# Kernel tuning notes

Hardware: AMD Instinct MI355X
Metric: run time of the kernel (lower is better)

Reference implementation:

```python
import jax, jax.numpy as jnp
import numpy as np

QUERY_SIZE = 512
KEY_SIZE = 512
VALUE_SIZE = 512
HIDDEN = 128


def setup_inputs() -> dict:
    key = jax.random.key(0)
    ks = jax.random.split(key, 9)
    b, t_q, t_k = 8, 128, 512
    query = jax.random.normal(ks[0], (b, t_q, QUERY_SIZE), dtype=jnp.float32)
    keys = jax.random.normal(ks[1], (b, t_k, KEY_SIZE), dtype=jnp.float32)
    values = jax.random.normal(ks[2], (b, t_k, VALUE_SIZE), dtype=jnp.float32)
    # torch nn.Linear init ~ U(-1/sqrt(fan_in), 1/sqrt(fan_in)); scale-matched normals are fine
    sq = 1.0 / np.sqrt(QUERY_SIZE)
    sk = 1.0 / np.sqrt(KEY_SIZE)
    sh = 1.0 / np.sqrt(HIDDEN)
    Wq = jax.random.uniform(ks[3], (HIDDEN, QUERY_SIZE), jnp.float32, -sq, sq)
    bq = jax.random.uniform(ks[4], (HIDDEN,), jnp.float32, -sq, sq)
    Wk = jax.random.uniform(ks[5], (HIDDEN, KEY_SIZE), jnp.float32, -sk, sk)
    bk = jax.random.uniform(ks[6], (HIDDEN,), jnp.float32, -sk, sk)
    Wo = jax.random.uniform(ks[7], (1, HIDDEN), jnp.float32, -sh, sh)
    bo = jax.random.uniform(ks[8], (1,), jnp.float32, -sh, sh)
    return {"query": query, "keys": keys, "values": values,
            "Wq": Wq, "bq": bq, "Wk": Wk, "bk": bk, "Wo": Wo, "bo": bo}


def reference(query, keys, values, Wq, bq, Wk, bk, Wo, bo):
    # Bahdanau additive attention: att_ij = Wo @ tanh(Wq q_i + Wk k_j + bq + bk) + bo
    # Project once per position (mathematically identical to the expanded per-pair Linear).
    q_proj = jnp.einsum('bqn,hn->bqh', query, Wq) + bq          # b x t_q x h
    k_proj = jnp.einsum('bkn,hn->bkh', keys, Wk) + bk           # b x t_k x h
    hid = jnp.tanh(q_proj[:, :, None, :] + k_proj[:, None, :, :])  # b x t_q x t_k x h
    scores = jnp.einsum('bqkh,h->bqk', hid, Wo[0]) + bo[0]       # b x t_q x t_k
    attn = jax.nn.softmax(scores, axis=2)
    context = jnp.einsum('bqk,bkv->bqv', attn, values)           # b x t_q x n_v
    return context, attn
```

## Files before the change

kernel.cpp:

```cpp
#include <hip/hip_runtime.h>


#define B_    8
#define TQ_   128
#define TK_   512
#define NIN_  512
#define H_    128
#define NV_   512
#define NQR   (B_*TQ_)
#define NROWS (NQR + B_*TK_)
#define CTXN  (B_*TQ_*NV_)

#define C2_   2.8853900817779268f
#define L2E_  1.4426950408889634f

__device__ __forceinline__ float fexp2(float x){ return __builtin_amdgcn_exp2f(x); }
__device__ __forceinline__ float frcp (float x){ return __builtin_amdgcn_rcpf(x); }

__global__ __launch_bounds__(256, 5) void proj_kernel(
        const float* __restrict__ query, const float* __restrict__ keys,
        const float* __restrict__ Wq, const float* __restrict__ Wk,
        float* __restrict__ psum, int kper) {
    __shared__ float at[32][18];
    __shared__ float wt[32][132];
    const int tid = threadIdx.x;
    const int r0  = blockIdx.x * 16;
    const float* in; const float* W;
    if (r0 < NQR) { in = query + (size_t)r0 * NIN_;         W = Wq; }
    else          { in = keys  + (size_t)(r0 - NQR) * NIN_; W = Wk; }

    const int r2 = (tid >> 5) * 2;
    const int h4 = (tid & 31) * 4;
    const int ar  = tid >> 4;
    const int ak2 = (tid & 15) * 2;
    const int wr  = tid >> 3;
    const int wkq = (tid & 7) * 4;
    const int kb0 = blockIdx.y * kper;
    const int nc  = kper >> 5;

    const float* pA  = in + (size_t)ar * NIN_ + kb0 + ak2;
    const float* pW0 = W + (size_t)(wr     ) * NIN_ + kb0 + wkq;
    const float* pW1 = W + (size_t)(wr + 32) * NIN_ + kb0 + wkq;
    const float* pW2 = W + (size_t)(wr + 64) * NIN_ + kb0 + wkq;
    const float* pW3 = W + (size_t)(wr + 96) * NIN_ + kb0 + wkq;

    float2 af = *(const float2*)pA;
    float4 w0 = *(const float4*)pW0, w1 = *(const float4*)pW1;
    float4 w2 = *(const float4*)pW2, w3 = *(const float4*)pW3;

    float acc[2][4] = {{0.f,0.f,0.f,0.f},{0.f,0.f,0.f,0.f}};

    for (int c = 0; c < nc; ++c) {
        __syncthreads();
        at[ak2+0][ar] = af.x; at[ak2+1][ar] = af.y;
        wt[wkq+0][wr   ] = w0.x; wt[wkq+1][wr   ] = w0.y;
        wt[wkq+2][wr   ] = w0.z; wt[wkq+3][wr   ] = w0.w;
        wt[wkq+0][wr+32] = w1.x; wt[wkq+1][wr+32] = w1.y;
        wt[wkq+2][wr+32] = w1.z; wt[wkq+3][wr+32] = w1.w;
        wt[wkq+0][wr+64] = w2.x; wt[wkq+1][wr+64] = w2.y;
        wt[wkq+2][wr+64] = w2.z; wt[wkq+3][wr+64] = w2.w;
        wt[wkq+0][wr+96] = w3.x; wt[wkq+1][wr+96] = w3.y;
        wt[wkq+2][wr+96] = w3.z; wt[wkq+3][wr+96] = w3.w;
        __syncthreads();
        if (c + 1 < nc) {
            pA += 32; pW0 += 32; pW1 += 32; pW2 += 32; pW3 += 32;
            af = *(const float2*)pA;
            w0 = *(const float4*)pW0; w1 = *(const float4*)pW1;
            w2 = *(const float4*)pW2; w3 = *(const float4*)pW3;
        }
#pragma unroll 8
        for (int kk = 0; kk < 32; ++kk) {
            const float2 a = *(const float2*)&at[kk][r2];
            const float4 w = *(const float4*)&wt[kk][h4];
            acc[0][0] = fmaf(a.x, w.x, acc[0][0]);
            acc[0][1] = fmaf(a.x, w.y, acc[0][1]);
            acc[0][2] = fmaf(a.x, w.z, acc[0][2]);
            acc[0][3] = fmaf(a.x, w.w, acc[0][3]);
            acc[1][0] = fmaf(a.y, w.x, acc[1][0]);
            acc[1][1] = fmaf(a.y, w.y, acc[1][1]);
            acc[1][2] = fmaf(a.y, w.z, acc[1][2]);
            acc[1][3] = fmaf(a.y, w.w, acc[1][3]);
        }
    }

    float* op = psum + ((size_t)blockIdx.y * NROWS + r0) * H_;
#pragma unroll
    for (int i = 0; i < 2; ++i) {
        float4 o = {acc[i][0], acc[i][1], acc[i][2], acc[i][3]};
        *(float4*)&op[(size_t)(r2 + i) * H_ + h4] = o;
    }
}

__global__ __launch_bounds__(256, 4) void reduceP_kernel(
        const float* __restrict__ psum, const float* __restrict__ bq,
        const float* __restrict__ bk, float* __restrict__ pout) {
    const int tid = threadIdx.x;
    const int r0  = blockIdx.x * 8;
    const float* bias = (r0 < NQR) ? bq : bk;
    const int row = tid >> 5, hq = (tid & 31) * 4;
    float4 s = *(const float4*)&bias[hq];
#pragma unroll
    for (int sp = 0; sp < 4; ++sp) {
        float4 v = *(const float4*)&psum[((size_t)sp * NROWS + r0 + row) * H_ + hq];
        s.x += v.x; s.y += v.y; s.z += v.z; s.w += v.w;
    }
    float4 o = {fexp2(s.x * C2_), fexp2(s.y * C2_),
                fexp2(s.z * C2_), fexp2(s.w * C2_)};
    *(float4*)&pout[(size_t)(r0 + row) * H_ + hq] = o;
}

__global__ __launch_bounds__(256, 4) void scores_kernel(
        const float* __restrict__ qe, const float* __restrict__ ke,
        const float* __restrict__ Wo, const float* __restrict__ bo,
        float* __restrict__ out_attn) {
    __shared__ float qs[2][H_];
    __shared__ float w2[H_];
    __shared__ float sc[2][TK_];

    const int tid = threadIdx.x;
    const int b   = blockIdx.y;
    const int q0  = blockIdx.x * 2;
    const int lane = tid & 63;

    qs[tid >> 7][tid & 127] =
        qe[(size_t)(b * TQ_ + q0 + (tid >> 7)) * H_ + (tid & 127)];
    if (tid < H_) w2[tid] = Wo[tid] * -2.0f;
    __syncthreads();

    float sw = w2[lane] + w2[lane + 64];
#pragma unroll
    for (int m = 1; m < 64; m <<= 1) sw += __shfl_xor(sw, m);
    const float sbase = bo[0] - 0.5f * sw;

#pragma unroll
    for (int half = 0; half < 2; ++half) {
        const int k = tid + half * 256;
        const float4* ke4 = (const float4*)&ke[(size_t)(b * TK_ + k) * H_];
        float s0 = 0.f, s1 = 0.f;
#pragma unroll 4
        for (int hb = 0; hb < 32; ++hb) {
            const float4 ek  = ke4[hb];
            const float4 wv  = *(const float4*)&w2[hb * 4];
            const float4 q0v = *(const float4*)&qs[0][hb * 4];
            const float4 q1v = *(const float4*)&qs[1][hb * 4];
            s0 = fmaf(wv.x, frcp(fmaf(q0v.x, ek.x, 1.f)), s0);
            s0 = fmaf(wv.y, frcp(fmaf(q0v.y, ek.y, 1.f)), s0);
            s0 = fmaf(wv.z, frcp(fmaf(q0v.z, ek.z, 1.f)), s0);
            s0 = fmaf(wv.w, frcp(fmaf(q0v.w, ek.w, 1.f)), s0);
            s1 = fmaf(wv.x, frcp(fmaf(q1v.x, ek.x, 1.f)), s1);
            s1 = fmaf(wv.y, frcp(fmaf(q1v.y, ek.y, 1.f)), s1);
            s1 = fmaf(wv.z, frcp(fmaf(q1v.z, ek.z, 1.f)), s1);
            s1 = fmaf(wv.w, frcp(fmaf(q1v.w, ek.w, 1.f)), s1);
        }
        sc[0][k] = s0 + sbase;
        sc[1][k] = s1 + sbase;
    }
    __syncthreads();

    const int w = tid >> 6;
    if (w < 2) {
        float4 sA = *(const float4*)&sc[w][lane * 8];
        float4 sB = *(const float4*)&sc[w][lane * 8 + 4];
        float m = fmaxf(fmaxf(fmaxf(sA.x, sA.y), fmaxf(sA.z, sA.w)),
                        fmaxf(fmaxf(sB.x, sB.y), fmaxf(sB.z, sB.w)));
#pragma unroll
        for (int mk = 1; mk < 64; mk <<= 1) m = fmaxf(m, __shfl_xor(m, mk));
        float4 eA, eB;
        eA.x = fexp2((sA.x - m) * L2E_); eA.y = fexp2((sA.y - m) * L2E_);
        eA.z = fexp2((sA.z - m) * L2E_); eA.w = fexp2((sA.w - m) * L2E_);
        eB.x = fexp2((sB.x - m) * L2E_); eB.y = fexp2((sB.y - m) * L2E_);
        eB.z = fexp2((sB.z - m) * L2E_); eB.w = fexp2((sB.w - m) * L2E_);
        float s = eA.x + eA.y + eA.z + eA.w + eB.x + eB.y + eB.z + eB.w;
#pragma unroll
        for (int mk = 1; mk < 64; mk <<= 1) s += __shfl_xor(s, mk);
        const float inv = frcp(s);
        eA.x *= inv; eA.y *= inv; eA.z *= inv; eA.w *= inv;
        eB.x *= inv; eB.y *= inv; eB.z *= inv; eB.w *= inv;
        float4* op = (float4*)&out_attn[(size_t)(b * TQ_ + q0 + w) * TK_ + lane * 8];
        op[0] = eA; op[1] = eB;
    }
}

__global__ __launch_bounds__(128, 4) void context_kernel(
        const float* __restrict__ attn, const float* __restrict__ values,
        float* __restrict__ psumC) {
    __shared__ float at[32][18];
    __shared__ float vt[32][68];

    const int tid = threadIdx.x;
    const int r0  = blockIdx.x * 16;
    const int b   = r0 >> 7;
    const int v0  = blockIdx.y * 64;
    const int kb0 = blockIdx.z * 128;

    const int q2 = (tid >> 4) * 2;
    const int v4 = (tid & 15) * 4;
    const int ar  = tid >> 3;
    const int akq = (tid & 7) * 4;
    const int vr  = tid >> 4;
    const int vq  = (tid & 15) * 4;

    const float* pAt = attn + (size_t)(r0 + ar) * TK_ + kb0 + akq;
    const float* pV0 = values + (size_t)(b * TK_ + kb0 + vr     ) * NV_ + v0 + vq;
    const float* pV1 = values + (size_t)(b * TK_ + kb0 + vr +  8) * NV_ + v0 + vq;
    const float* pV2 = values + (size_t)(b * TK_ + kb0 + vr + 16) * NV_ + v0 + vq;
    const float* pV3 = values + (size_t)(b * TK_ + kb0 + vr + 24) * NV_ + v0 + vq;

    float4 af  = *(const float4*)pAt;
    float4 vf0 = *(const float4*)pV0;
    float4 vf1 = *(const float4*)pV1;
    float4 vf2 = *(const float4*)pV2;
    float4 vf3 = *(const float4*)pV3;

    float acc[2][4] = {{0.f,0.f,0.f,0.f},{0.f,0.f,0.f,0.f}};

    for (int c = 0; c < 4; ++c) {
        __syncthreads();
        at[akq+0][ar] = af.x; at[akq+1][ar] = af.y;
        at[akq+2][ar] = af.z; at[akq+3][ar] = af.w;
        *(float4*)&vt[vr     ][vq] = vf0;
        *(float4*)&vt[vr +  8][vq] = vf1;
        *(float4*)&vt[vr + 16][vq] = vf2;
        *(float4*)&vt[vr + 24][vq] = vf3;
        __syncthreads();
        if (c + 1 < 4) {
            pAt += 32; pV0 += 32 * NV_; pV1 += 32 * NV_;
            pV2 += 32 * NV_; pV3 += 32 * NV_;
            af  = *(const float4*)pAt;
            vf0 = *(const float4*)pV0; vf1 = *(const float4*)pV1;
            vf2 = *(const float4*)pV2; vf3 = *(const float4*)pV3;
        }
#pragma unroll 8
        for (int kk = 0; kk < 32; ++kk) {
            const float2 a = *(const float2*)&at[kk][q2];
            const float4 v = *(const float4*)&vt[kk][v4];
            acc[0][0] = fmaf(a.x, v.x, acc[0][0]);
            acc[0][1] = fmaf(a.x, v.y, acc[0][1]);
            acc[0][2] = fmaf(a.x, v.z, acc[0][2]);
            acc[0][3] = fmaf(a.x, v.w, acc[0][3]);
            acc[1][0] = fmaf(a.y, v.x, acc[1][0]);
            acc[1][1] = fmaf(a.y, v.y, acc[1][1]);
            acc[1][2] = fmaf(a.y, v.z, acc[1][2]);
            acc[1][3] = fmaf(a.y, v.w, acc[1][3]);
        }
    }

    float* op = psumC + (size_t)blockIdx.z * CTXN + (size_t)r0 * NV_ + v0;
#pragma unroll
    for (int i = 0; i < 2; ++i) {
        float4 o = {acc[i][0], acc[i][1], acc[i][2], acc[i][3]};
        *(float4*)&op[(size_t)(q2 + i) * NV_ + v4] = o;
    }
}

__global__ __launch_bounds__(256, 4) void reduceC_kernel(
        const float* __restrict__ psumC, float* __restrict__ outc) {
    const size_t i = ((size_t)blockIdx.x * 256 + threadIdx.x) * 4;
    float4 s = *(const float4*)&psumC[i];
#pragma unroll
    for (int z = 1; z < 4; ++z) {
        float4 v = *(const float4*)&psumC[(size_t)z * CTXN + i];
        s.x += v.x; s.y += v.y; s.z += v.z; s.w += v.w;
    }
    *(float4*)&outc[i] = s;
}

extern "C" void kernel_launch(void* const* d_in, const int* in_sizes, int n_in,
                              void* d_out, int out_size, void* d_ws, size_t ws_size,
                              hipStream_t stream) {
    const float* query  = (const float*)d_in[0];
    const float* keys   = (const float*)d_in[1];
    const float* values = (const float*)d_in[2];
    const float* Wq     = (const float*)d_in[3];
    const float* bq     = (const float*)d_in[4];
    const float* Wk     = (const float*)d_in[5];
    const float* bk     = (const float*)d_in[6];
    const float* Wo     = (const float*)d_in[7];
    const float* bo     = (const float*)d_in[8];

    float* out_ctx  = (float*)d_out;
    float* out_attn = out_ctx + B_ * TQ_ * NV_;
    float* pout  = (float*)d_ws;
    float* qe    = pout;
    float* ke    = pout + (size_t)NQR * H_;
    float* psumP = pout + (size_t)NROWS * H_;
    float* psumC = psumP + (size_t)4 * NROWS * H_;

    proj_kernel<<<dim3(NROWS / 16, 4), 256, 0, stream>>>(
        query, keys, Wq, Wk, psumP, NIN_ / 4);
    reduceP_kernel<<<NROWS / 8, 256, 0, stream>>>(psumP, bq, bk, pout);
    scores_kernel<<<dim3(TQ_ / 2, B_), 256, 0, stream>>>(qe, ke, Wo, bo, out_attn);
    context_kernel<<<dim3(NQR / 16, NV_ / 64, 4), 128, 0, stream>>>(
        out_attn, values, psumC);
    reduceC_kernel<<<CTXN / 1024, 256, 0, stream>>>(psumC, out_ctx);
}
```

Baseline: 63.45 us.

## Enlarge proj register tile and split scores to one query per block

The projection GEMM now runs 128 threads per block. Each thread computes a 4x4 output tile instead of 2x4, and loads float4 from both A and W, which raises arithmetic intensity per shared-memory load. The scores kernel now handles one query per block with twice as many blocks. Each thread scores two keys with vector accumulators, and the softmax uses a block-wide reduction through a small shared array instead of a staged score buffer. The extra blocks add parallelism, but ke rows are now reread per query, since keys are no longer shared across two queries.

```diff
diff --git a/kernel.cpp b/kernel.cpp
--- a/kernel.cpp
+++ b/kernel.cpp
@@ -17,11 +17,11 @@
 __device__ __forceinline__ float fexp2(float x){ return __builtin_amdgcn_exp2f(x); }
 __device__ __forceinline__ float frcp (float x){ return __builtin_amdgcn_rcpf(x); }
 
-__global__ __launch_bounds__(256, 5) void proj_kernel(
+__global__ __launch_bounds__(128, 4) void proj_kernel(
         const float* __restrict__ query, const float* __restrict__ keys,
         const float* __restrict__ Wq, const float* __restrict__ Wk,
         float* __restrict__ psum, int kper) {
-    __shared__ float at[32][18];
+    __shared__ float at[32][20];
     __shared__ float wt[32][132];
     const int tid = threadIdx.x;
     const int r0  = blockIdx.x * 16;
@@ -29,65 +29,84 @@
     if (r0 < NQR) { in = query + (size_t)r0 * NIN_;         W = Wq; }
     else          { in = keys  + (size_t)(r0 - NQR) * NIN_; W = Wk; }
 
-    const int r2 = (tid >> 5) * 2;
+    const int r4 = (tid >> 5) * 4;
     const int h4 = (tid & 31) * 4;
-    const int ar  = tid >> 4;
-    const int ak2 = (tid & 15) * 2;
-    const int wr  = tid >> 3;
-    const int wkq = (tid & 7) * 4;
+    const int sr  = tid >> 3;
+    const int skq = (tid & 7) * 4;
     const int kb0 = blockIdx.y * kper;
     const int nc  = kper >> 5;
 
-    const float* pA  = in + (size_t)ar * NIN_ + kb0 + ak2;
-    const float* pW0 = W + (size_t)(wr     ) * NIN_ + kb0 + wkq;
-    const float* pW1 = W + (size_t)(wr + 32) * NIN_ + kb0 + wkq;
-    const float* pW2 = W + (size_t)(wr + 64) * NIN_ + kb0 + wkq;
-    const float* pW3 = W + (size_t)(wr + 96) * NIN_ + kb0 + wkq;
-
-    float2 af = *(const float2*)pA;
+    const float* pA  = in + (size_t)sr * NIN_ + kb0 + skq;
+    const float* pW0 = W + (size_t)(sr      ) * NIN_ + kb0 + skq;
+    const float* pW1 = W + (size_t)(sr + 16 ) * NIN_ + kb0 + skq;
+    const float* pW2 = W + (size_t)(sr + 32 ) * NIN_ + kb0 + skq;
+    const float* pW3 = W + (size_t)(sr + 48 ) * NIN_ + kb0 + skq;
+    const float* pW4 = W + (size_t)(sr + 64 ) * NIN_ + kb0 + skq;
+    const float* pW5 = W + (size_t)(sr + 80 ) * NIN_ + kb0 + skq;
+    const float* pW6 = W + (size_t)(sr + 96 ) * NIN_ + kb0 + skq;
+    const float* pW7 = W + (size_t)(sr + 112) * NIN_ + kb0 + skq;
+
+    float4 af = *(const float4*)pA;
     float4 w0 = *(const float4*)pW0, w1 = *(const float4*)pW1;
     float4 w2 = *(const float4*)pW2, w3 = *(const float4*)pW3;
-
-    float acc[2][4] = {{0.f,0.f,0.f,0.f},{0.f,0.f,0.f,0.f}};
+    float4 w4 = *(const float4*)pW4, w5 = *(const float4*)pW5;
+    float4 w6 = *(const float4*)pW6, w7 = *(const float4*)pW7;
+
+    float acc[4][4];
+#pragma unroll
+    for (int i = 0; i < 4; ++i)
+#pragma unroll
+        for (int j = 0; j < 4; ++j) acc[i][j] = 0.0f;
 
     for (int c = 0; c < nc; ++c) {
         __syncthreads();
-        at[ak2+0][ar] = af.x; at[ak2+1][ar] = af.y;
-        wt[wkq+0][wr   ] = w0.x; wt[wkq+1][wr   ] = w0.y;
-        wt[wkq+2][wr   ] = w0.z; wt[wkq+3][wr   ] = w0.w;
-        wt[wkq+0][wr+32] = w1.x; wt[wkq+1][wr+32] = w1.y;
-        wt[wkq+2][wr+32] = w1.z; wt[wkq+3][wr+32] = w1.w;
-        wt[wkq+0][wr+64] = w2.x; wt[wkq+1][wr+64] = w2.y;
-        wt[wkq+2][wr+64] = w2.z; wt[wkq+3][wr+64] = w2.w;
-        wt[wkq+0][wr+96] = w3.x; wt[wkq+1][wr+96] = w3.y;
-        wt[wkq+2][wr+96] = w3.z; wt[wkq+3][wr+96] = w3.w;
+        at[skq+0][sr] = af.x; at[skq+1][sr] = af.y;
+        at[skq+2][sr] = af.z; at[skq+3][sr] = af.w;
+        wt[skq+0][sr    ] = w0.x; wt[skq+1][sr    ] = w0.y;
+        wt[skq+2][sr    ] = w0.z; wt[skq+3][sr    ] = w0.w;
+        wt[skq+0][sr+ 16] = w1.x; wt[skq+1][sr+ 16] = w1.y;
+        wt[skq+2][sr+ 16] = w1.z; wt[skq+3][sr+ 16] = w1.w;
+        wt[skq+0][sr+ 32] = w2.x; wt[skq+1][sr+ 32] = w2.y;
+        wt[skq+2][sr+ 32] = w2.z; wt[skq+3][sr+ 32] = w2.w;
+        wt[skq+0][sr+ 48] = w3.x; wt[skq+1][sr+ 48] = w3.y;
+        wt[skq+2][sr+ 48] = w3.z; wt[skq+3][sr+ 48] = w3.w;
+        wt[skq+0][sr+ 64] = w4.x; wt[skq+1][sr+ 64] = w4.y;
+        wt[skq+2][sr+ 64] = w4.z; wt[skq+3][sr+ 64] = w4.w;
+        wt[skq+0][sr+ 80] = w5.x; wt[skq+1][sr+ 80] = w5.y;
+        wt[skq+2][sr+ 80] = w5.z; wt[skq+3][sr+ 80] = w5.w;
+        wt[skq+0][sr+ 96] = w6.x; wt[skq+1][sr+ 96] = w6.y;
+        wt[skq+2][sr+ 96] = w6.z; wt[skq+3][sr+ 96] = w6.w;
+        wt[skq+0][sr+112] = w7.x; wt[skq+1][sr+112] = w7.y;
+        wt[skq+2][sr+112] = w7.z; wt[skq+3][sr+112] = w7.w;
         __syncthreads();
         if (c + 1 < nc) {
             pA += 32; pW0 += 32; pW1 += 32; pW2 += 32; pW3 += 32;
-            af = *(const float2*)pA;
+            pW4 += 32; pW5 += 32; pW6 += 32; pW7 += 32;
+            af = *(const float4*)pA;
             w0 = *(const float4*)pW0; w1 = *(const float4*)pW1;
             w2 = *(const float4*)pW2; w3 = *(const float4*)pW3;
+            w4 = *(const float4*)pW4; w5 = *(const float4*)pW5;
+            w6 = *(const float4*)pW6; w7 = *(const float4*)pW7;
         }
 #pragma unroll 8
         for (int kk = 0; kk < 32; ++kk) {
-            const float2 a = *(const float2*)&at[kk][r2];
+            const float4 a = *(const float4*)&at[kk][r4];
             const float4 w = *(const float4*)&wt[kk][h4];
-            acc[0][0] = fmaf(a.x, w.x, acc[0][0]);
-            acc[0][1] = fmaf(a.x, w.y, acc[0][1]);
-            acc[0][2] = fmaf(a.x, w.z, acc[0][2]);
-            acc[0][3] = fmaf(a.x, w.w, acc[0][3]);
-            acc[1][0] = fmaf(a.y, w.x, acc[1][0]);
-            acc[1][1] = fmaf(a.y, w.y, acc[1][1]);
-            acc[1][2] = fmaf(a.y, w.z, acc[1][2]);
-            acc[1][3] = fmaf(a.y, w.w, acc[1][3]);
+            const float av[4] = {a.x, a.y, a.z, a.w};
+            const float wv[4] = {w.x, w.y, w.z, w.w};
+#pragma unroll
+            for (int i = 0; i < 4; ++i)
+#pragma unroll
+                for (int j = 0; j < 4; ++j)
+                    acc[i][j] = fmaf(av[i], wv[j], acc[i][j]);
         }
     }
 
     float* op = psum + ((size_t)blockIdx.y * NROWS + r0) * H_;
 #pragma unroll
-    for (int i = 0; i < 2; ++i) {
+    for (int i = 0; i < 4; ++i) {
         float4 o = {acc[i][0], acc[i][1], acc[i][2], acc[i][3]};
-        *(float4*)&op[(size_t)(r2 + i) * H_ + h4] = o;
+        *(float4*)&op[(size_t)(r4 + i) * H_ + h4] = o;
     }
 }
 
@@ -113,18 +132,18 @@
         const float* __restrict__ qe, const float* __restrict__ ke,
         const float* __restrict__ Wo, const float* __restrict__ bo,
         float* __restrict__ out_attn) {
-    __shared__ float qs[2][H_];
+    __shared__ float qs[H_];
     __shared__ float w2[H_];
-    __shared__ float sc[2][TK_];
-
-    const int tid = threadIdx.x;
-    const int b   = blockIdx.y;
-    const int q0  = blockIdx.x * 2;
+    __shared__ float red[8];
+
+    const int tid  = threadIdx.x;
+    const int b    = blockIdx.y;
+    const int q    = blockIdx.x;
     const int lane = tid & 63;
-
-    qs[tid >> 7][tid & 127] =
-        qe[(size_t)(b * TQ_ + q0 + (tid >> 7)) * H_ + (tid & 127)];
-    if (tid < H_) w2[tid] = Wo[tid] * -2.0f;
+    const int w    = tid >> 6;
+
+    if (tid < 128) qs[tid] = qe[(size_t)(b * TQ_ + q) * H_ + tid];
+    else           w2[tid - 128] = Wo[tid - 128] * -2.0f;
     __syncthreads();
 
     float sw = w2[lane] + w2[lane + 64];
@@ -132,53 +151,47 @@
     for (int m = 1; m < 64; m <<= 1) sw += __shfl_xor(sw, m);
     const float sbase = bo[0] - 0.5f * sw;
 
-#pragma unroll
-    for (int half = 0; half < 2; ++half) {
-        const int k = tid + half * 256;
-        const float4* ke4 = (const float4*)&ke[(size_t)(b * TK_ + k) * H_];
-        float s0 = 0.f, s1 = 0.f;
+    const float4* ke0 = (const float4*)&ke[(size_t)(b * TK_ + tid      ) * H_];
+    const float4* ke1 = (const float4*)&ke[(size_t)(b * TK_ + tid + 256) * H_];
+    float4 a0 = {0.f,0.f,0.f,0.f}, a1 = {0.f,0.f,0.f,0.f};
 #pragma unroll 4
-        for (int hb = 0; hb < 32; ++hb) {
-            const float4 ek  = ke4[hb];
-            const float4 wv  = *(const float4*)&w2[hb * 4];
-            const float4 q0v = *(const float4*)&qs[0][hb * 4];
-            const float4 q1v = *(const float4*)&qs[1][hb * 4];
-            s0 = fmaf(wv.x, frcp(fmaf(q0v.x, ek.x, 1.f)), s0);
-            s0 = fmaf(wv.y, frcp(fmaf(q0v.y, ek.y, 1.f)), s0);
-            s0 = fmaf(wv.z, frcp(fmaf(q0v.z, ek.z, 1.f)), s0);
-            s0 = fmaf(wv.w, frcp(fmaf(q0v.w, ek.w, 1.f)), s0);
-            s1 = fmaf(wv.x, frcp(fmaf(q1v.x, ek.x, 1.f)), s1);
-            s1 = fmaf(wv.y, frcp(fmaf(q1v.y, ek.y, 1.f)), s1);
-            s1 = fmaf(wv.z, frcp(fmaf(q1v.z, ek.z, 1.f)), s1);
-            s1 = fmaf(wv.w, frcp(fmaf(q1v.w, ek.w, 1.f)), s1);
-        }
-        sc[0][k] = s0 + sbase;
-        sc[1][k] = s1 + sbase;
-    }
+    for (int hb = 0; hb < 32; ++hb) {
+        const float4 e0 = ke0[hb];
+        const float4 e1 = ke1[hb];
+        const float4 wv = *(const float4*)&w2[hb * 4];
+        const float4 qv = *(const float4*)&qs[hb * 4];
+        a0.x = fmaf(wv.x, frcp(fmaf(qv.x, e0.x, 1.f)), a0.x);
+        a0.y = fmaf(wv.y, frcp(fmaf(qv.y, e0.y, 1.f)), a0.y);
+        a0.z = fmaf(wv.z, frcp(fmaf(qv.z, e0.z, 1.f)), a0.z);
+        a0.w = fmaf(wv.w, frcp(fmaf(qv.w, e0.w, 1.f)), a0.w);
+        a1.x = fmaf(wv.x, frcp(fmaf(qv.x, e1.x, 1.f)), a1.x);
+        a1.y = fmaf(wv.y, frcp(fmaf(qv.y, e1.y, 1.f)), a1.y);
+        a1.z = fmaf(wv.z, frcp(fmaf(qv.z, e1.z, 1.f)), a1.z);
+        a1.w = fmaf(wv.w, frcp(fmaf(qv.w, e1.w, 1.f)), a1.w);
+    }
+    const float s0 = (a0.x + a0.y) + (a0.z + a0.w) + sbase;
+    const float s1 = (a1.x + a1.y) + (a1.z + a1.w) + sbase;
+
+    float mx = fmaxf(s0, s1);
+#pragma unroll
+    for (int m = 1; m < 64; m <<= 1) mx = fmaxf(mx, __shfl_xor(mx, m));
+    if (lane == 0) red[w] = mx;
     __syncthreads();
-
-    const int w = tid >> 6;
-    if (w < 2) {
-        float4 sA = *(const float4*)&sc[w][lane * 8];
-        float4 sB = *(const float4*)&sc[w][lane * 8 + 4];
-        float m = fmaxf(fmaxf(fmaxf(sA.x, sA.y), fmaxf(sA.z, sA.w)),
-                        fmaxf(fmaxf(sB.x, sB.y), fmaxf(sB.z, sB.w)));
-#pragma unroll
-        for (int mk = 1; mk < 64; mk <<= 1) m = fmaxf(m, __shfl_xor(m, mk));
-        float4 eA, eB;
-        eA.x = fexp2((sA.x - m) * L2E_); eA.y = fexp2((sA.y - m) * L2E_);
-        eA.z = fexp2((sA.z - m) * L2E_); eA.w = fexp2((sA.w - m) * L2E_);
-        eB.x = fexp2((sB.x - m) * L2E_); eB.y = fexp2((sB.y - m) * L2E_);
-        eB.z = fexp2((sB.z - m) * L2E_); eB.w = fexp2((sB.w - m) * L2E_);
-        float s = eA.x + eA.y + eA.z + eA.w + eB.x + eB.y + eB.z + eB.w;
-#pragma unroll
-        for (int mk = 1; mk < 64; mk <<= 1) s += __shfl_xor(s, mk);
-        const float inv = frcp(s);
-        eA.x *= inv; eA.y *= inv; eA.z *= inv; eA.w *= inv;
-        eB.x *= inv; eB.y *= inv; eB.z *= inv; eB.w *= inv;
-        float4* op = (float4*)&out_attn[(size_t)(b * TQ_ + q0 + w) * TK_ + lane * 8];
-        op[0] = eA; op[1] = eB;
-    }
+    mx = fmaxf(fmaxf(red[0], red[1]), fmaxf(red[2], red[3]));
+
+    const float e0 = fexp2((s0 - mx) * L2E_);
+    const float e1 = fexp2((s1 - mx) * L2E_);
+    float sum = e0 + e1;
+#pragma unroll
+    for (int m = 1; m < 64; m <<= 1) sum += __shfl_xor(sum, m);
+    if (lane == 0) red[4 + w] = sum;
+    __syncthreads();
+    sum = (red[4] + red[5]) + (red[6] + red[7]);
+    const float inv = frcp(sum);
+
+    float* op = &out_attn[(size_t)(b * TQ_ + q) * TK_];
+    op[tid]       = e0 * inv;
+    op[tid + 256] = e1 * inv;
 }
 
 __global__ __launch_bounds__(128, 4) void context_kernel(
@@ -286,10 +299,10 @@
     float* psumP = pout + (size_t)NROWS * H_;
     float* psumC = psumP + (size_t)4 * NROWS * H_;
 
-    proj_kernel<<<dim3(NROWS / 16, 4), 256, 0, stream>>>(
+    proj_kernel<<<dim3(NROWS / 16, 4), 128, 0, stream>>>(
         query, keys, Wq, Wk, psumP, NIN_ / 4);
     reduceP_kernel<<<NROWS / 8, 256, 0, stream>>>(psumP, bq, bk, pout);
-    scores_kernel<<<dim3(TQ_ / 2, B_), 256, 0, stream>>>(qe, ke, Wo, bo, out_attn);
+    scores_kernel<<<dim3(TQ_, B_), 256, 0, stream>>>(qe, ke, Wo, bo, out_attn);
     context_kernel<<<dim3(NQR / 16, NV_ / 64, 4), 128, 0, stream>>>(
         out_attn, values, psumC);
     reduceC_kernel<<<CTXN / 1024, 256, 0, stream>>>(psumC, out_ctx);
```

Measured after the change: 77.06 us. 1.21x slower.

## Transpose key projections to h-major layout for coalesced score loads

Applied to the files above, without the earlier changes.

The reduce kernel now writes the exponentiated key projections transposed (batch × hidden × t_k) through a shared-memory tile, while query projections stay row-major. The scores kernel then has each thread compute four adjacent keys for one query, reading contiguous float4s across keys. Before, each thread walked its own key row, which gave strided per-lane accesses. This gives coalesced global loads and reuses each key load across four accumulators, at the cost of losing the per-thread reuse of one key vector across two queries and adding a transpose step in the reduce.

```diff
diff --git a/kernel.cpp b/kernel.cpp
--- a/kernel.cpp
+++ b/kernel.cpp
@@ -93,24 +93,50 @@
 
 __global__ __launch_bounds__(256, 4) void reduceP_kernel(
         const float* __restrict__ psum, const float* __restrict__ bq,
-        const float* __restrict__ bk, float* __restrict__ pout) {
+        const float* __restrict__ bk, float* __restrict__ qe,
+        float* __restrict__ keT) {
+    __shared__ float lt[128][17];
     const int tid = threadIdx.x;
-    const int r0  = blockIdx.x * 8;
-    const float* bias = (r0 < NQR) ? bq : bk;
-    const int row = tid >> 5, hq = (tid & 31) * 4;
-    float4 s = *(const float4*)&bias[hq];
-#pragma unroll
-    for (int sp = 0; sp < 4; ++sp) {
-        float4 v = *(const float4*)&psum[((size_t)sp * NROWS + r0 + row) * H_ + hq];
-        s.x += v.x; s.y += v.y; s.z += v.z; s.w += v.w;
-    }
-    float4 o = {fexp2(s.x * C2_), fexp2(s.y * C2_),
-                fexp2(s.z * C2_), fexp2(s.w * C2_)};
-    *(float4*)&pout[(size_t)(r0 + row) * H_ + hq] = o;
+    const int r0  = blockIdx.x * 16;
+    const bool isq = (r0 < NQR);
+    const float* bias = isq ? bq : bk;
+
+#pragma unroll
+    for (int p = 0; p < 2; ++p) {
+        const int j = tid + p * 256;
+        const int row = j >> 5, hq = (j & 31) * 4;
+        float4 s = *(const float4*)&bias[hq];
+#pragma unroll
+        for (int sp = 0; sp < 4; ++sp) {
+            const float4 v = *(const float4*)
+                &psum[((size_t)sp * NROWS + r0 + row) * H_ + hq];
+            s.x += v.x; s.y += v.y; s.z += v.z; s.w += v.w;
+        }
+        float4 e = {fexp2(s.x * C2_), fexp2(s.y * C2_),
+                    fexp2(s.z * C2_), fexp2(s.w * C2_)};
+        if (isq) {
+            *(float4*)&qe[(size_t)(r0 + row) * H_ + hq] = e;
+        } else {
+            lt[hq + 0][row] = e.x; lt[hq + 1][row] = e.y;
+            lt[hq + 2][row] = e.z; lt[hq + 3][row] = e.w;
+        }
+    }
+    if (!isq) {
+        __syncthreads();
+        const int b  = (r0 - NQR) >> 9;
+        const int k0 = (r0 - NQR) & 511;
+#pragma unroll
+        for (int p = 0; p < 2; ++p) {
+            const int j = tid + p * 256;
+            const int h = j >> 2, kq = (j & 3) * 4;
+            float4 o = {lt[h][kq], lt[h][kq + 1], lt[h][kq + 2], lt[h][kq + 3]};
+            *(float4*)&keT[((size_t)b * H_ + h) * TK_ + k0 + kq] = o;
+        }
+    }
 }
 
 __global__ __launch_bounds__(256, 4) void scores_kernel(
-        const float* __restrict__ qe, const float* __restrict__ ke,
+        const float* __restrict__ qe, const float* __restrict__ keT,
         const float* __restrict__ Wo, const float* __restrict__ bo,
         float* __restrict__ out_attn) {
     __shared__ float qs[2][H_];
@@ -132,29 +158,23 @@
     for (int m = 1; m < 64; m <<= 1) sw += __shfl_xor(sw, m);
     const float sbase = bo[0] - 0.5f * sw;
 
-#pragma unroll
-    for (int half = 0; half < 2; ++half) {
-        const int k = tid + half * 256;
-        const float4* ke4 = (const float4*)&ke[(size_t)(b * TK_ + k) * H_];
-        float s0 = 0.f, s1 = 0.f;
+    const int k4 = (tid & 127) * 4;
+    const int qi = tid >> 7;
+    const float* pk = keT + (size_t)b * H_ * TK_ + k4;
+    float a0 = 0.f, a1 = 0.f, a2 = 0.f, a3 = 0.f;
 #pragma unroll 4
-        for (int hb = 0; hb < 32; ++hb) {
-            const float4 ek  = ke4[hb];
-            const float4 wv  = *(const float4*)&w2[hb * 4];
-            const float4 q0v = *(const float4*)&qs[0][hb * 4];
-            const float4 q1v = *(const float4*)&qs[1][hb * 4];
-            s0 = fmaf(wv.x, frcp(fmaf(q0v.x, ek.x, 1.f)), s0);
-            s0 = fmaf(wv.y, frcp(fmaf(q0v.y, ek.y, 1.f)), s0);
-            s0 = fmaf(wv.z, frcp(fmaf(q0v.z, ek.z, 1.f)), s0);
-            s0 = fmaf(wv.w, frcp(fmaf(q0v.w, ek.w, 1.f)), s0);
-            s1 = fmaf(wv.x, frcp(fmaf(q1v.x, ek.x, 1.f)), s1);
-            s1 = fmaf(wv.y, frcp(fmaf(q1v.y, ek.y, 1.f)), s1);
-            s1 = fmaf(wv.z, frcp(fmaf(q1v.z, ek.z, 1.f)), s1);
-            s1 = fmaf(wv.w, frcp(fmaf(q1v.w, ek.w, 1.f)), s1);
-        }
-        sc[0][k] = s0 + sbase;
-        sc[1][k] = s1 + sbase;
-    }
+    for (int h = 0; h < H_; ++h) {
+        const float4 ek = *(const float4*)pk;
+        pk += TK_;
+        const float qv = qs[qi][h];
+        const float wv = w2[h];
+        a0 = fmaf(wv, frcp(fmaf(qv, ek.x, 1.f)), a0);
+        a1 = fmaf(wv, frcp(fmaf(qv, ek.y, 1.f)), a1);
+        a2 = fmaf(wv, frcp(fmaf(qv, ek.z, 1.f)), a2);
+        a3 = fmaf(wv, frcp(fmaf(qv, ek.w, 1.f)), a3);
+    }
+    float4 sv = {a0 + sbase, a1 + sbase, a2 + sbase, a3 + sbase};
+    *(float4*)&sc[qi][k4] = sv;
     __syncthreads();
 
     const int w = tid >> 6;
@@ -282,14 +302,14 @@
     float* out_attn = out_ctx + B_ * TQ_ * NV_;
     float* pout  = (float*)d_ws;
     float* qe    = pout;
-    float* ke    = pout + (size_t)NQR * H_;
+    float* keT   = pout + (size_t)NQR * H_;
     float* psumP = pout + (size_t)NROWS * H_;
     float* psumC = psumP + (size_t)4 * NROWS * H_;
 
     proj_kernel<<<dim3(NROWS / 16, 4), 256, 0, stream>>>(
         query, keys, Wq, Wk, psumP, NIN_ / 4);
-    reduceP_kernel<<<NROWS / 8, 256, 0, stream>>>(psumP, bq, bk, pout);
-    scores_kernel<<<dim3(TQ_ / 2, B_), 256, 0, stream>>>(qe, ke, Wo, bo, out_attn);
+    reduceP_kernel<<<NROWS / 16, 256, 0, stream>>>(psumP, bq, bk, qe, keT);
+    scores_kernel<<<dim3(TQ_ / 2, B_), 256, 0, stream>>>(qe, keT, Wo, bo, out_attn);
     context_kernel<<<dim3(NQR / 16, NV_ / 64, 4), 128, 0, stream>>>(
         out_attn, values, psumC);
     reduceC_kernel<<<CTXN / 1024, 256, 0, stream>>>(psumC, out_ctx);
```

After: 60.62 us. 1.05x faster.
